# Kernel tuning notes

Hardware: AMD Instinct MI355X
Metric: run time of the kernel (lower is better)

The kernel has to match this reference:

```python
import jax, jax.numpy as jnp
import numpy as np

IN_F = 4096
OUT_F = 4096
B, S = 4, 2048
RMS_EPS = 1e-6
Q_EPS = 1e-5


def setup_inputs() -> dict:
    key = jax.random.key(0)
    kx, kw, kb, ks = jax.random.split(key, 4)
    x = jax.random.normal(kx, (B, S, IN_F), dtype=jnp.float32)
    # ternary BitNet weight in {-1, 0, +1}, stored as float32 for the reference
    W = (jax.random.randint(kw, (OUT_F, IN_F), 0, 3) - 1).astype(jnp.float32)
    rms_weight = jnp.ones((IN_F,), dtype=jnp.float32)
    bias = jax.random.normal(kb, (OUT_F,), dtype=jnp.float32)
    weight_scale = jax.random.uniform(ks, (1,), dtype=jnp.float32) + 0.5
    return {"x": x, "W": W, "rms_weight": rms_weight, "bias": bias,
            "weight_scale": weight_scale}


def reference(x, W, rms_weight, bias, weight_scale):
    # RMSNorm (self.rms_norm applied before quantized matmul)
    var = jnp.mean(x * x, axis=-1, keepdims=True)
    h = x * jax.lax.rsqrt(var + RMS_EPS) * rms_weight
    # BitNet act_quant: per-token absmax int8 quantization
    scale = 127.0 / jnp.clip(jnp.max(jnp.abs(h), axis=-1, keepdims=True), Q_EPS)  # [B,S,1]
    q = jnp.clip(jnp.round(h * scale), -128.0, 127.0)
    # ternary GEMV per token, then dequant
    y = jnp.einsum('bsk,ok->bso', q, W) / scale  # [B,S,OUT_F]
    y = y + bias
    y = y * weight_scale  # weight_scale_mode == 'multiply'
    return y
```

## Files before the change

kernel.cpp:

```cpp
#include <hip/hip_runtime.h>

#define IN_F 4096
#define OUT_F 4096
#define NTOK 8192
#define KDIM 4096

using i32x4 = __attribute__((ext_vector_type(4))) int;
using f32x4 = __attribute__((ext_vector_type(4))) float;

__device__ __forceinline__ void gload_lds16(const void* g, void* l) {
  __builtin_amdgcn_global_load_lds(
      (const __attribute__((address_space(1))) void*)g,
      (__attribute__((address_space(3))) void*)l, 16, 0, 0);
}

__global__ __launch_bounds__(256) void rmsq_kernel(
    const float* __restrict__ x, const float* __restrict__ rmsw,
    signed char* __restrict__ q, float* __restrict__ dscale) {
  const int tok = blockIdx.x;
  const int tid = threadIdx.x;
  const f32x4* xr = (const f32x4*)(x + (size_t)tok * IN_F);
  const f32x4* wr = (const f32x4*)rmsw;

  f32x4 v[4];
  float ss = 0.f;
#pragma unroll
  for (int c = 0; c < 4; ++c) {
    v[c] = xr[c * 256 + tid];
    ss += v[c].x * v[c].x + v[c].y * v[c].y + v[c].z * v[c].z + v[c].w * v[c].w;
  }

  __shared__ float red[4];
#pragma unroll
  for (int off = 32; off > 0; off >>= 1) ss += __shfl_down(ss, off, 64);
  const int wid = tid >> 6;
  if ((tid & 63) == 0) red[wid] = ss;
  __syncthreads();
  const float tot = red[0] + red[1] + red[2] + red[3];
  const float rinv = rsqrtf(tot * (1.0f / IN_F) + 1e-6f);

  f32x4 h[4];
  float amax = 0.f;
#pragma unroll
  for (int c = 0; c < 4; ++c) {
    f32x4 w = wr[c * 256 + tid];
    h[c].x = v[c].x * rinv * w.x;
    h[c].y = v[c].y * rinv * w.y;
    h[c].z = v[c].z * rinv * w.z;
    h[c].w = v[c].w * rinv * w.w;
    amax = fmaxf(amax, fabsf(h[c].x));
    amax = fmaxf(amax, fabsf(h[c].y));
    amax = fmaxf(amax, fabsf(h[c].z));
    amax = fmaxf(amax, fabsf(h[c].w));
  }

  __syncthreads();
#pragma unroll
  for (int off = 32; off > 0; off >>= 1)
    amax = fmaxf(amax, __shfl_down(amax, off, 64));
  if ((tid & 63) == 0) red[wid] = amax;
  __syncthreads();
  amax = fmaxf(fmaxf(red[0], red[1]), fmaxf(red[2], red[3]));
  amax = fmaxf(amax, 1e-5f);
  const float qs = 127.0f / amax;
  if (tid == 0) dscale[tok] = amax * (1.0f / 127.0f);

  uint* qo = (uint*)(q + (size_t)tok * IN_F);
#pragma unroll
  for (int c = 0; c < 4; ++c) {
    float r0 = fminf(fmaxf(rintf(h[c].x * qs), -128.f), 127.f);
    float r1 = fminf(fmaxf(rintf(h[c].y * qs), -128.f), 127.f);
    float r2 = fminf(fmaxf(rintf(h[c].z * qs), -128.f), 127.f);
    float r3 = fminf(fmaxf(rintf(h[c].w * qs), -128.f), 127.f);
    uint p = ((uint)((int)r0 & 255)) | ((uint)((int)r1 & 255) << 8) |
             ((uint)((int)r2 & 255) << 16) | ((uint)((int)r3 & 255) << 24);
    qo[c * 256 + tid] = p;
  }
}

__global__ __launch_bounds__(256) void wconv_kernel(
    const float* __restrict__ W, signed char* __restrict__ Wq) {
  const int idx = blockIdx.x * 256 + threadIdx.x;
  f32x4 w = ((const f32x4*)W)[idx];
  uint p = ((uint)((int)w.x & 255)) | ((uint)((int)w.y & 255) << 8) |
           ((uint)((int)w.z & 255) << 16) | ((uint)((int)w.w & 255) << 24);
  ((uint*)Wq)[idx] = p;
}

#define BM 128
#define BN 128
#define BK 64

__global__ __launch_bounds__(256) void gemm_kernel(
    const signed char* __restrict__ A, const signed char* __restrict__ Bw,
    const float* __restrict__ dscale, const float* __restrict__ bias,
    const float* __restrict__ wscale_p, float* __restrict__ out) {
  __shared__ signed char As[BM * BK];
  __shared__ signed char Bs[BN * BK];

  const int tid = threadIdx.x;
  const int lane = tid & 63;
  const int wid = tid >> 6;
  const int wr = wid >> 1;
  const int wc = wid & 1;
  const int m0 = blockIdx.x * BM;
  const int n0 = blockIdx.y * BN;

  i32x4 acc[4][4];
#pragma unroll
  for (int i = 0; i < 4; ++i)
#pragma unroll
    for (int j = 0; j < 4; ++j) acc[i][j] = (i32x4){0, 0, 0, 0};

  const int srow = tid >> 2;
  const int scol = (tid & 3) * 16;
  const signed char* Ag = A + (size_t)(m0 + srow) * KDIM + scol;
  const signed char* Bg = Bw + (size_t)(n0 + srow) * KDIM + scol;

  const int kgrp = (lane >> 4) * 16;
  const int fr = lane & 15;

  for (int k0 = 0; k0 < KDIM; k0 += BK) {
    gload_lds16(Ag + k0, &As[tid * 16]);
    gload_lds16(Ag + k0 + (size_t)64 * KDIM, &As[tid * 16 + 4096]);
    gload_lds16(Bg + k0, &Bs[tid * 16]);
    gload_lds16(Bg + k0 + (size_t)64 * KDIM, &Bs[tid * 16 + 4096]);
    __syncthreads();

    i32x4 af[4], bf[4];
#pragma unroll
    for (int mi = 0; mi < 4; ++mi)
      af[mi] = *(const i32x4*)&As[(wr * 64 + mi * 16 + fr) * BK + kgrp];
#pragma unroll
    for (int ni = 0; ni < 4; ++ni)
      bf[ni] = *(const i32x4*)&Bs[(wc * 64 + ni * 16 + fr) * BK + kgrp];

#pragma unroll
    for (int mi = 0; mi < 4; ++mi)
#pragma unroll
      for (int ni = 0; ni < 4; ++ni)
        acc[mi][ni] = __builtin_amdgcn_mfma_i32_16x16x64_i8(af[mi], bf[ni],
                                                            acc[mi][ni], 0, 0, 0);
    __syncthreads();
  }

  const float wsc = wscale_p[0];
  const int rbase = (lane >> 4) * 4;
#pragma unroll
  for (int mi = 0; mi < 4; ++mi) {
#pragma unroll
    for (int r = 0; r < 4; ++r) {
      const int m = m0 + wr * 64 + mi * 16 + rbase + r;
      const float ds = dscale[m];
      float* orow = out + (size_t)m * OUT_F + n0 + wc * 64;
#pragma unroll
      for (int ni = 0; ni < 4; ++ni) {
        const int n = ni * 16 + fr;
        orow[n] = ((float)acc[mi][ni][r] * ds + bias[n0 + wc * 64 + n]) * wsc;
      }
    }
  }
}

extern "C" void kernel_launch(void* const* d_in, const int* in_sizes, int n_in,
                              void* d_out, int out_size, void* d_ws, size_t ws_size,
                              hipStream_t stream) {
  const float* x = (const float*)d_in[0];
  const float* W = (const float*)d_in[1];
  const float* rmsw = (const float*)d_in[2];
  const float* bias = (const float*)d_in[3];
  const float* wscale = (const float*)d_in[4];
  float* out = (float*)d_out;

  signed char* q = (signed char*)d_ws;
  signed char* Wq = q + (size_t)NTOK * IN_F;
  float* dscale = (float*)(Wq + (size_t)OUT_F * IN_F);

  rmsq_kernel<<<NTOK, 256, 0, stream>>>(x, rmsw, q, dscale);
  wconv_kernel<<<(OUT_F * IN_F / 4) / 256, 256, 0, stream>>>(W, Wq);
  gemm_kernel<<<dim3(NTOK / BM, OUT_F / BN), 256, 0, stream>>>(q, Wq, dscale,
                                                               bias, wscale, out);
}
```

Before: 215.8 us.

## Rework int8 GEMM with 256x256 tiles, triple-buffered async LDS, swizzle

The int8 MFMA GEMM moves to 256x256 block tiles with 512 threads. It keeps three LDS stages filled by async global_load_lds, using vmcnt waits and raw barriers so later loads overlap with current MFMA work. An XOR swizzle on LDS rows is meant to cut bank conflicts, and a grid remap improves L2 locality. Bias is hoisted into registers and MFMA issue gets a priority bump. The cost is higher register and LDS use (96KB LDS with 2 blocks per CU requested), and the pipeline depends on correct waitcnt counting.

Measured after the change: 195.5 us. 1.1x faster.

```diff
diff --git a/kernel.cpp b/kernel.cpp
--- a/kernel.cpp
+++ b/kernel.cpp
@@ -13,6 +13,10 @@
       (const __attribute__((address_space(1))) void*)g,
       (__attribute__((address_space(3))) void*)l, 16, 0, 0);
 }
+
+#define WAITV(n) asm volatile("s_waitcnt vmcnt(" #n ")" ::: "memory")
+#define BAR() do { asm volatile("" ::: "memory"); __builtin_amdgcn_s_barrier(); \
+                   asm volatile("" ::: "memory"); } while (0)
 
 __global__ __launch_bounds__(256) void rmsq_kernel(
     const float* __restrict__ x, const float* __restrict__ rmsw,
@@ -87,79 +91,121 @@
   ((uint*)Wq)[idx] = p;
 }
 
-#define BM 128
-#define BN 128
+#define BM 256
+#define BN 256
 #define BK 64
-
-__global__ __launch_bounds__(256) void gemm_kernel(
+#define NT (KDIM / BK)
+#define ABYTES (BM * BK)
+#define BUFBYTES (2 * ABYTES)
+
+__global__ __launch_bounds__(512, 2) void gemm_kernel(
     const signed char* __restrict__ A, const signed char* __restrict__ Bw,
     const float* __restrict__ dscale, const float* __restrict__ bias,
     const float* __restrict__ wscale_p, float* __restrict__ out) {
-  __shared__ signed char As[BM * BK];
-  __shared__ signed char Bs[BN * BK];
+  __shared__ __align__(16) signed char lds[3 * BUFBYTES];
 
   const int tid = threadIdx.x;
   const int lane = tid & 63;
   const int wid = tid >> 6;
-  const int wr = wid >> 1;
-  const int wc = wid & 1;
-  const int m0 = blockIdx.x * BM;
-  const int n0 = blockIdx.y * BN;
-
-  i32x4 acc[4][4];
-#pragma unroll
-  for (int i = 0; i < 4; ++i)
+  const int wr = wid >> 2;
+  const int wc = wid & 3;
+
+  const int bid = blockIdx.x;
+  const int swz = (bid & 7) * 64 + (bid >> 3);
+  const int m0 = (swz & 31) * BM;
+  const int n0 = (swz >> 5) * BN;
+
+  const int cA0 = tid, cA1 = tid + 512;
+  const int rA0 = cA0 >> 2, rA1 = cA1 >> 2;
+  const int sA0 = (cA0 & 3) ^ ((rA0 >> 1) & 3);
+  const int sA1 = (cA1 & 3) ^ ((rA1 >> 1) & 3);
+  const signed char* agp0 = A + (size_t)(m0 + rA0) * KDIM + sA0 * 16;
+  const signed char* agp1 = A + (size_t)(m0 + rA1) * KDIM + sA1 * 16;
+  const signed char* bgp0 = Bw + (size_t)(n0 + rA0) * KDIM + sA0 * 16;
+  const signed char* bgp1 = Bw + (size_t)(n0 + rA1) * KDIM + sA1 * 16;
+
+#define STAGE(kt, bufb)                                                    \
+  do {                                                                     \
+    const int k0_ = (kt) * BK;                                             \
+    signed char* lb_ = &lds[(bufb)];                                       \
+    gload_lds16(agp0 + k0_, lb_ + cA0 * 16);                               \
+    gload_lds16(agp1 + k0_, lb_ + cA1 * 16);                               \
+    gload_lds16(bgp0 + k0_, lb_ + ABYTES + cA0 * 16);                      \
+    gload_lds16(bgp1 + k0_, lb_ + ABYTES + cA1 * 16);                      \
+  } while (0)
+
+  const int fr = lane & 15;
+  const int ks = lane >> 4;
+  int offA[8], offB[4];
+#pragma unroll
+  for (int mi = 0; mi < 8; ++mi) {
+    const int row = wr * 128 + mi * 16 + fr;
+    offA[mi] = row * BK + ((ks ^ ((row >> 1) & 3)) * 16);
+  }
+#pragma unroll
+  for (int ni = 0; ni < 4; ++ni) {
+    const int row = wc * 64 + ni * 16 + fr;
+    offB[ni] = ABYTES + row * BK + ((ks ^ ((row >> 1) & 3)) * 16);
+  }
+
+  i32x4 acc[8][4];
+#pragma unroll
+  for (int i = 0; i < 8; ++i)
 #pragma unroll
     for (int j = 0; j < 4; ++j) acc[i][j] = (i32x4){0, 0, 0, 0};
 
-  const int srow = tid >> 2;
-  const int scol = (tid & 3) * 16;
-  const signed char* Ag = A + (size_t)(m0 + srow) * KDIM + scol;
-  const signed char* Bg = Bw + (size_t)(n0 + srow) * KDIM + scol;
-
-  const int kgrp = (lane >> 4) * 16;
-  const int fr = lane & 15;
-
-  for (int k0 = 0; k0 < KDIM; k0 += BK) {
-    gload_lds16(Ag + k0, &As[tid * 16]);
-    gload_lds16(Ag + k0 + (size_t)64 * KDIM, &As[tid * 16 + 4096]);
-    gload_lds16(Bg + k0, &Bs[tid * 16]);
-    gload_lds16(Bg + k0 + (size_t)64 * KDIM, &Bs[tid * 16 + 4096]);
-    __syncthreads();
-
-    i32x4 af[4], bf[4];
-#pragma unroll
-    for (int mi = 0; mi < 4; ++mi)
-      af[mi] = *(const i32x4*)&As[(wr * 64 + mi * 16 + fr) * BK + kgrp];
-#pragma unroll
-    for (int ni = 0; ni < 4; ++ni)
-      bf[ni] = *(const i32x4*)&Bs[(wc * 64 + ni * 16 + fr) * BK + kgrp];
-
-#pragma unroll
-    for (int mi = 0; mi < 4; ++mi)
+  STAGE(0, 0);
+  STAGE(1, BUFBYTES);
+  STAGE(2, 2 * BUFBYTES);
+
+  int bufb = 0;
+  for (int t = 0; t < NT; ++t) {
+    if (t < NT - 2)       WAITV(8);
+    else if (t == NT - 2) WAITV(4);
+    else                  WAITV(0);
+    BAR();
+
+    const signed char* bp = &lds[bufb];
+    i32x4 af[8], bf[4];
+#pragma unroll
+    for (int mi = 0; mi < 8; ++mi) af[mi] = *(const i32x4*)(bp + offA[mi]);
+#pragma unroll
+    for (int ni = 0; ni < 4; ++ni) bf[ni] = *(const i32x4*)(bp + offB[ni]);
+
+    __builtin_amdgcn_s_setprio(1);
+#pragma unroll
+    for (int mi = 0; mi < 8; ++mi)
 #pragma unroll
       for (int ni = 0; ni < 4; ++ni)
         acc[mi][ni] = __builtin_amdgcn_mfma_i32_16x16x64_i8(af[mi], bf[ni],
                                                             acc[mi][ni], 0, 0, 0);
-    __syncthreads();
+    __builtin_amdgcn_s_setprio(0);
+    BAR();
+
+    if (t + 3 < NT) STAGE(t + 3, bufb);
+    bufb += BUFBYTES;
+    if (bufb == 3 * BUFBYTES) bufb = 0;
   }
 
   const float wsc = wscale_p[0];
   const int rbase = (lane >> 4) * 4;
-#pragma unroll
-  for (int mi = 0; mi < 4; ++mi) {
+  float bv[4];
+#pragma unroll
+  for (int ni = 0; ni < 4; ++ni) bv[ni] = bias[n0 + wc * 64 + ni * 16 + fr];
+#pragma unroll
+  for (int mi = 0; mi < 8; ++mi) {
 #pragma unroll
     for (int r = 0; r < 4; ++r) {
-      const int m = m0 + wr * 64 + mi * 16 + rbase + r;
+      const int m = m0 + wr * 128 + mi * 16 + rbase + r;
       const float ds = dscale[m];
       float* orow = out + (size_t)m * OUT_F + n0 + wc * 64;
 #pragma unroll
       for (int ni = 0; ni < 4; ++ni) {
-        const int n = ni * 16 + fr;
-        orow[n] = ((float)acc[mi][ni][r] * ds + bias[n0 + wc * 64 + n]) * wsc;
+        orow[ni * 16 + fr] = ((float)acc[mi][ni][r] * ds + bv[ni]) * wsc;
       }
     }
   }
+#undef STAGE
 }
 
 extern "C" void kernel_launch(void* const* d_in, const int* in_sizes, int n_in,
@@ -178,6 +224,6 @@
 
   rmsq_kernel<<<NTOK, 256, 0, stream>>>(x, rmsw, q, dscale);
   wconv_kernel<<<(OUT_F * IN_F / 4) / 256, 256, 0, stream>>>(W, Wq);
-  gemm_kernel<<<dim3(NTOK / BM, OUT_F / BN), 256, 0, stream>>>(q, Wq, dscale,
-                                                               bias, wscale, out);
-}
+  gemm_kernel<<<(NTOK / BM) * (OUT_F / BN), 512, 0, stream>>>(q, Wq, dscale,
+                                                              bias, wscale, out);
+}
```
